# Kernel optimization log

Hardware: AMD Instinct MI355X
Metric: run time of the kernel (lower is better)

## Reference

```python
import jax, jax.numpy as jnp
import numpy as np

N_NODES = 100000
N_EDGES = 1600000
D_IN = 256
D_OUT = 256


def setup_inputs() -> dict:
    key = jax.random.key(0)
    k1, k2, k3, k4, k5 = jax.random.split(key, 5)
    feat = jax.random.normal(k1, (N_NODES, D_IN), dtype=jnp.float32)
    src = jax.random.randint(k2, (N_EDGES,), 0, N_NODES, dtype=jnp.int32)
    dst = jax.random.randint(k3, (N_EDGES,), 0, N_NODES, dtype=jnp.int32)
    # xavier_uniform with gain for relu (sqrt(2)), as in reset_parameters
    gain = float(np.sqrt(2.0))
    limit = gain * float(np.sqrt(6.0 / (D_IN + D_OUT)))
    w_neigh = jax.random.uniform(k4, (D_OUT, D_IN), minval=-limit, maxval=limit, dtype=jnp.float32)
    w_self = jax.random.uniform(k5, (D_OUT, D_IN), minval=-limit, maxval=limit, dtype=jnp.float32)
    b_self = jnp.zeros((D_OUT,), dtype=jnp.float32)
    return {"feat": feat, "src": src, "dst": dst,
            "w_neigh": w_neigh, "w_self": w_self, "b_self": b_self}


def reference(feat, src, dst, w_neigh, w_self, b_self):
    # SAGEConv, aggregator_type='mean', feat_drop=0, no edge_weight.
    # lin_before_mp = (in_feats > out_feats) = False -> aggregate raw feats first.
    n = feat.shape[0]
    # gather messages at edges and segment-sum into dst nodes
    summed = jax.ops.segment_sum(feat[src], dst, num_segments=n)  # [N, D_in]
    deg = jax.ops.segment_sum(jnp.ones_like(dst, dtype=feat.dtype), dst, num_segments=n)
    h_neigh_raw = summed / jnp.maximum(deg, 1.0)[:, None]  # mean; 0 for isolated nodes
    h_neigh = h_neigh_raw @ w_neigh.T                       # fc_neigh (no bias)
    rst = feat @ w_self.T + b_self + h_neigh                # fc_self(h_self) + h_neigh
    return rst
```

## Files before the change

kernel.cpp:

```cpp
#include <hip/hip_runtime.h>
#include <cstddef>

#define N_NODES 100000
#define N_EDGES 1600000
#define D 256

typedef short          s16x8 __attribute__((ext_vector_type(8)));
typedef unsigned short u16x8 __attribute__((ext_vector_type(8)));
typedef float          f32x4 __attribute__((ext_vector_type(4)));
typedef float          f32x8 __attribute__((ext_vector_type(8)));

__device__ __forceinline__ unsigned short f2bf(float f) {
    unsigned int u = __float_as_uint(f);
    unsigned int r = (u + 0x7fffu + ((u >> 16) & 1u)) >> 16;
    return (unsigned short)r;
}
__device__ __forceinline__ float bf2f(unsigned short u) {
    return __uint_as_float(((unsigned int)u) << 16);
}

#define WS_COUNTS 0
#define WS_ROWPTR (N_NODES)
#define WS_COL    (2 * N_NODES + 16)
#define WS_PART   (WS_COL + N_EDGES)
#define WB_BYTE   ((size_t)(WS_PART + 128) * 4)
#define FB_BYTE   (WB_BYTE + 2 * 65536 * 2)
#define FB_SZ     ((size_t)N_NODES * D * 2)
#define FQ_BYTE   FB_BYTE
#define FQ_SZ     ((size_t)N_NODES * D)
#define HB3_BYTE  (FQ_BYTE + FQ_SZ)
#define NEED_XL3  (HB3_BYTE + FB_SZ)
#define NEED_LARGE (FB_BYTE + FB_SZ)
#define NEED_MID  (FB_BYTE)

#define EBLOCKS ((N_EDGES + 255) / 256)
#define FBLOCKS (N_NODES * D / 8 / 256)
#define SCAN_NB ((N_NODES + 1023) / 1024)
#define GEMMBLKS ((N_NODES + 63) / 64)

__global__ __launch_bounds__(256) void cvt_hist_u8_kernel(
    const float* __restrict__ feat, const float* __restrict__ w_self,
    const float* __restrict__ w_neigh, const int* __restrict__ dst,
    unsigned char* __restrict__ fq, unsigned short* __restrict__ wb,
    int* __restrict__ counts)
{
    const int b = blockIdx.x;
    if (b < FBLOCKS) {
        const int i = b * 256 + threadIdx.x;
        const f32x8 v = ((const f32x8*)feat)[i];
        unsigned int p0 = 0, p1 = 0;
#pragma unroll
        for (int k = 0; k < 4; ++k) {
            int q = (int)rintf(fminf(fmaxf(v[k] * 16.0f, -127.0f), 127.0f)) + 128;
            p0 |= ((unsigned int)q) << (8 * k);
        }
#pragma unroll
        for (int k = 0; k < 4; ++k) {
            int q = (int)rintf(fminf(fmaxf(v[4 + k] * 16.0f, -127.0f), 127.0f)) + 128;
            p1 |= ((unsigned int)q) << (8 * k);
        }
        uint2 o; o.x = p0; o.y = p1;
        *(uint2*)(fq + (size_t)i * 8) = o;
    } else if (b < FBLOCKS + 128) {
        const int i = (b - FBLOCKS) * 256 + threadIdx.x;
        const bool isself = (i < 16384);
        const float* srcp = isself ? w_self : w_neigh;
        const int j = (isself ? i : i - 16384) * 4;
        const float4 v = *(const float4*)(srcp + j);
        ushort4 o;
        o.x = f2bf(v.x); o.y = f2bf(v.y); o.z = f2bf(v.z); o.w = f2bf(v.w);
        ((ushort4*)wb)[i] = o;
    } else {
        const int i = (b - FBLOCKS - 128) * 256 + threadIdx.x;
        if (i < N_EDGES) atomicAdd(&counts[dst[i]], 1);
    }
}

__global__ __launch_bounds__(256) void cvt_hist_bf16_kernel(
    const float* __restrict__ feat, const float* __restrict__ w_self,
    const float* __restrict__ w_neigh, const int* __restrict__ dst,
    unsigned short* __restrict__ fb, unsigned short* __restrict__ wb,
    int* __restrict__ counts)
{
    const int b = blockIdx.x;
    if (b < FBLOCKS) {
        const int i = b * 256 + threadIdx.x;
        const f32x8 v = ((const f32x8*)feat)[i];
        ushort4 a, c;
        a.x = f2bf(v[0]); a.y = f2bf(v[1]); a.z = f2bf(v[2]); a.w = f2bf(v[3]);
        c.x = f2bf(v[4]); c.y = f2bf(v[5]); c.z = f2bf(v[6]); c.w = f2bf(v[7]);
        ((ushort4*)fb)[i * 2 + 0] = a;
        ((ushort4*)fb)[i * 2 + 1] = c;
    } else if (b < FBLOCKS + 128) {
        const int i = (b - FBLOCKS) * 256 + threadIdx.x;
        const bool isself = (i < 16384);
        const float* srcp = isself ? w_self : w_neigh;
        const int j = (isself ? i : i - 16384) * 4;
        const float4 v = *(const float4*)(srcp + j);
        ushort4 o;
        o.x = f2bf(v.x); o.y = f2bf(v.y); o.z = f2bf(v.z); o.w = f2bf(v.w);
        ((ushort4*)wb)[i] = o;
    } else {
        const int i = (b - FBLOCKS - 128) * 256 + threadIdx.x;
        if (i < N_EDGES) atomicAdd(&counts[dst[i]], 1);
    }
}

__global__ __launch_bounds__(256) void wcvt_hist_kernel(
    const float* __restrict__ w_self, const float* __restrict__ w_neigh,
    const int* __restrict__ dst, unsigned short* __restrict__ wb,
    int* __restrict__ counts)
{
    const int b = blockIdx.x;
    if (b < 128) {
        const int i = b * 256 + threadIdx.x;
        const bool isself = (i < 16384);
        const float* srcp = isself ? w_self : w_neigh;
        const int j = (isself ? i : i - 16384) * 4;
        const float4 v = *(const float4*)(srcp + j);
        ushort4 o;
        o.x = f2bf(v.x); o.y = f2bf(v.y); o.z = f2bf(v.z); o.w = f2bf(v.w);
        ((ushort4*)wb)[i] = o;
    } else {
        const int i = (b - 128) * 256 + threadIdx.x;
        if (i < N_EDGES) atomicAdd(&counts[dst[i]], 1);
    }
}

__global__ __launch_bounds__(1024) void scan_block_kernel(
    const int* __restrict__ counts, int* __restrict__ row_ptr,
    int* __restrict__ partials)
{
    __shared__ int wsum[16];
    const int t = threadIdx.x, b = blockIdx.x, i = b * 1024 + t;
    const int lane = t & 63, w = t >> 6;
    int x = (i < N_NODES) ? counts[i] : 0;
#pragma unroll
    for (int off = 1; off < 64; off <<= 1) {
        int y = __shfl_up(x, off, 64);
        if (lane >= off) x += y;
    }
    if (lane == 63) wsum[w] = x;
    __syncthreads();
    if (w == 0) {
        int s = (lane < 16) ? wsum[lane] : 0;
#pragma unroll
        for (int off = 1; off < 16; off <<= 1) {
            int y = __shfl_up(s, off, 64);
            if (lane >= off) s += y;
        }
        if (lane < 16) wsum[lane] = s;
    }
    __syncthreads();
    const int incl = x + (w > 0 ? wsum[w - 1] : 0);
    if (i < N_NODES) row_ptr[i + 1] = incl;
    if (t == 1023) partials[b] = incl;
}

__global__ __launch_bounds__(1024) void scan_add2_kernel(
    const int* __restrict__ partials, int* __restrict__ row_ptr)
{
    __shared__ int sp[SCAN_NB];
    const int t = threadIdx.x, b = blockIdx.x;
    if (t < SCAN_NB) sp[t] = partials[t];
    __syncthreads();
    int off = 0;
    for (int j = 0; j < b; ++j) off += sp[j];
    const int i = b * 1024 + t;
    if (i < N_NODES) row_ptr[i + 1] += off;
    if (b == 0 && t == 0) row_ptr[0] = 0;
}

__global__ __launch_bounds__(256) void fill_kernel(
    const int* __restrict__ src, const int* __restrict__ dst,
    const int* __restrict__ row_ptr, int* __restrict__ counts,
    int* __restrict__ col)
{
    const int i = blockIdx.x * 256 + threadIdx.x;
    if (i < N_EDGES) {
        const int d = dst[i];
        const int pos = atomicSub(&counts[d], 1) - 1;
        col[row_ptr[d] + pos] = src[i];
    }
}

__global__ __launch_bounds__(256) void aggregate4_kernel(
    const unsigned char* __restrict__ fq,
    const int* __restrict__ row_ptr, const int* __restrict__ col,
    unsigned short* __restrict__ hb)
{
    const int node = (blockIdx.x * blockDim.x + threadIdx.x) >> 6;
    const int lane = threadIdx.x & 63;
    if (node >= N_NODES) return;
    const int beg = row_ptr[node], end = row_ptr[node + 1];
    const int quarter = lane >> 4;
    const int chunk = lane & 15;

    unsigned int aE[4] = {0,0,0,0}, aO[4] = {0,0,0,0};
    unsigned int bE[4] = {0,0,0,0}, bO[4] = {0,0,0,0};
    const unsigned char* base = fq + chunk * 16;

    int j = beg + quarter;
    for (; j + 4 < end; j += 8) {
        const int s0 = col[j];
        const int s1 = col[j + 4];
        const uint4 u = *(const uint4*)(base + (size_t)s0 * D);
        const uint4 v = *(const uint4*)(base + (size_t)s1 * D);
        aE[0] += u.x & 0x00FF00FFu;  aO[0] += (u.x >> 8) & 0x00FF00FFu;
        aE[1] += u.y & 0x00FF00FFu;  aO[1] += (u.y >> 8) & 0x00FF00FFu;
        aE[2] += u.z & 0x00FF00FFu;  aO[2] += (u.z >> 8) & 0x00FF00FFu;
        aE[3] += u.w & 0x00FF00FFu;  aO[3] += (u.w >> 8) & 0x00FF00FFu;
        bE[0] += v.x & 0x00FF00FFu;  bO[0] += (v.x >> 8) & 0x00FF00FFu;
        bE[1] += v.y & 0x00FF00FFu;  bO[1] += (v.y >> 8) & 0x00FF00FFu;
        bE[2] += v.z & 0x00FF00FFu;  bO[2] += (v.z >> 8) & 0x00FF00FFu;
        bE[3] += v.w & 0x00FF00FFu;  bO[3] += (v.w >> 8) & 0x00FF00FFu;
    }
    for (; j < end; j += 4) {
        const int s0 = col[j];
        const uint4 u = *(const uint4*)(base + (size_t)s0 * D);
        aE[0] += u.x & 0x00FF00FFu;  aO[0] += (u.x >> 8) & 0x00FF00FFu;
        aE[1] += u.y & 0x00FF00FFu;  aO[1] += (u.y >> 8) & 0x00FF00FFu;
        aE[2] += u.z & 0x00FF00FFu;  aO[2] += (u.z >> 8) & 0x00FF00FFu;
        aE[3] += u.w & 0x00FF00FFu;  aO[3] += (u.w >> 8) & 0x00FF00FFu;
    }

#pragma unroll
    for (int d = 0; d < 4; ++d) {
        unsigned int e = aE[d] + bE[d];
        unsigned int o = aO[d] + bO[d];
        e += __shfl_xor((int)e, 16, 64);
        e += __shfl_xor((int)e, 32, 64);
        o += __shfl_xor((int)o, 16, 64);
        o += __shfl_xor((int)o, 32, 64);
        aE[d] = e; aO[d] = o;
    }

    if (quarter == 0) {
        const int deg = end - beg;
        const float inv = 1.0f / (16.0f * fmaxf((float)deg, 1.0f));
        const float bias = 128.0f * (float)deg;
        u16x8 o0, o1;
#pragma unroll
        for (int d = 0; d < 4; ++d) {
            const float e0 = ((float)(aE[d] & 0xFFFFu) - bias) * inv;
            const float e2 = ((float)(aE[d] >> 16)     - bias) * inv;
            const float e1 = ((float)(aO[d] & 0xFFFFu) - bias) * inv;
            const float e3 = ((float)(aO[d] >> 16)     - bias) * inv;
            if (d < 2) {
                o0[d * 4 + 0] = f2bf(e0); o0[d * 4 + 1] = f2bf(e1);
                o0[d * 4 + 2] = f2bf(e2); o0[d * 4 + 3] = f2bf(e3);
            } else {
                o1[(d - 2) * 4 + 0] = f2bf(e0); o1[(d - 2) * 4 + 1] = f2bf(e1);
                o1[(d - 2) * 4 + 2] = f2bf(e2); o1[(d - 2) * 4 + 3] = f2bf(e3);
            }
        }
        unsigned short* op = hb + (size_t)node * D + chunk * 16;
        *(u16x8*)op = o0;
        *(u16x8*)(op + 8) = o1;
    }
}

__global__ __launch_bounds__(256) void gemm_v4_kernel(
    const float* __restrict__ feat,
    const unsigned short* __restrict__ hb,
    const unsigned short* __restrict__ wb,
    const float* __restrict__ b_self,
    float* __restrict__ outp)
{
    __shared__ unsigned short As[64 * 64];

    const int t    = threadIdx.x;
    const int lane = t & 63;
    const int w    = t >> 6;
    const int row0 = blockIdx.x * 64;
    const int c0   = w * 64;
    const int nl   = lane & 15;
    const int kg   = lane >> 4;

    const int tr = t >> 2;
    const int tq = t & 3;
    int grow = row0 + tr; if (grow > N_NODES - 1) grow = N_NODES - 1;
    const size_t gf = (size_t)grow * D;

    int wsw[2];
#pragma unroll
    for (int c = 0; c < 2; ++c) {
        const int cs = tq * 16 + c * 8;
        wsw[c] = tr * 64 + (cs ^ ((tr & 7) << 3));
    }
    int rsw[4][2];
#pragma unroll
    for (int m = 0; m < 4; ++m) {
        const int r = m * 16 + nl;
#pragma unroll
        for (int kk = 0; kk < 2; ++kk) {
            const int cs = kg * 8 + kk * 32;
            rsw[m][kk] = r * 64 + (cs ^ ((r & 7) << 3));
        }
    }

    f32x4 acc[4][4];
#pragma unroll
    for (int m = 0; m < 4; ++m)
#pragma unroll
        for (int n = 0; n < 4; ++n) acc[m][n] = (f32x4){0.f, 0.f, 0.f, 0.f};

    f32x8 stf0, stf1;
    u16x8 sth0, sth1;
    stf0 = *(const f32x8*)(feat + gf + tq * 16);
    stf1 = *(const f32x8*)(feat + gf + tq * 16 + 8);

#pragma unroll
    for (int s = 0; s < 8; ++s) {
        u16x8 w0, w1;
        if (s < 4) {
#pragma unroll
            for (int i = 0; i < 8; ++i) { w0[i] = f2bf(stf0[i]); w1[i] = f2bf(stf1[i]); }
        } else {
            w0 = sth0; w1 = sth1;
        }
        *(u16x8*)&As[wsw[0]] = w0;
        *(u16x8*)&As[wsw[1]] = w1;
        __syncthreads();

        if (s + 1 < 4) {
            const int koff = (s + 1) * 64 + tq * 16;
            stf0 = *(const f32x8*)(feat + gf + koff);
            stf1 = *(const f32x8*)(feat + gf + koff + 8);
        } else if (s + 1 < 8) {
            const int koff = ((s + 1) & 3) * 64 + tq * 16;
            sth0 = *(const u16x8*)(hb + gf + koff);
            sth1 = *(const u16x8*)(hb + gf + koff + 8);
        }

        const int hsel = (s < 4) ? 0 : 65536;
        const int kbase = (s & 3) * 64;
#pragma unroll
        for (int kk = 0; kk < 2; ++kk) {
            s16x8 a[4], b[4];
#pragma unroll
            for (int m = 0; m < 4; ++m)
                a[m] = *(const s16x8*)&As[rsw[m][kk]];
#pragma unroll
            for (int n = 0; n < 4; ++n)
                b[n] = *(const s16x8*)(wb + hsel
                        + (size_t)(c0 + n * 16 + nl) * 256 + kbase + kk * 32 + kg * 8);
#pragma unroll
            for (int m = 0; m < 4; ++m)
#pragma unroll
                for (int n = 0; n < 4; ++n)
                    acc[m][n] = __builtin_amdgcn_mfma_f32_16x16x32_bf16(
                        a[m], b[n], acc[m][n], 0, 0, 0);
        }
        __syncthreads();
    }

#pragma unroll
    for (int n = 0; n < 4; ++n) {
        const float bias = b_self[c0 + n * 16 + nl];
#pragma unroll
        for (int m = 0; m < 4; ++m) {
            const int rbase = row0 + m * 16 + kg * 4;
#pragma unroll
            for (int r = 0; r < 4; ++r) {
                const int row = rbase + r;
                if (row < N_NODES)
                    outp[(size_t)row * D + c0 + n * 16 + nl] = acc[m][n][r] + bias;
            }
        }
    }
}

__global__ __launch_bounds__(256) void aggregate2f_kernel(
    const unsigned short* __restrict__ featb,
    const int* __restrict__ row_ptr, const int* __restrict__ col,
    float* __restrict__ outf)
{
    const int node = (blockIdx.x * blockDim.x + threadIdx.x) >> 6;
    const int lane = threadIdx.x & 63;
    if (node >= N_NODES) return;
    const int beg = row_ptr[node], end = row_ptr[node + 1];
    const int half = lane >> 5;
    const int chunk = lane & 31;

    float a0[8] = {0,0,0,0,0,0,0,0};
    float a1[8] = {0,0,0,0,0,0,0,0};
    float a2[8] = {0,0,0,0,0,0,0,0};
    float a3[8] = {0,0,0,0,0,0,0,0};
    const unsigned short* fbp = featb + chunk * 8;

    int j = beg + half;
    for (; j + 6 < end; j += 8) {
        const int s0 = col[j], s1 = col[j + 2], s2 = col[j + 4], s3 = col[j + 6];
        const u16x8 u0 = *(const u16x8*)(fbp + (size_t)s0 * D);
        const u16x8 u1 = *(const u16x8*)(fbp + (size_t)s1 * D);
        const u16x8 u2 = *(const u16x8*)(fbp + (size_t)s2 * D);
        const u16x8 u3 = *(const u16x8*)(fbp + (size_t)s3 * D);
#pragma unroll
        for (int i = 0; i < 8; ++i) a0[i] += bf2f(u0[i]);
#pragma unroll
        for (int i = 0; i < 8; ++i) a1[i] += bf2f(u1[i]);
#pragma unroll
        for (int i = 0; i < 8; ++i) a2[i] += bf2f(u2[i]);
#pragma unroll
        for (int i = 0; i < 8; ++i) a3[i] += bf2f(u3[i]);
    }
    for (; j < end; j += 2) {
        const int s0 = col[j];
        const u16x8 u0 = *(const u16x8*)(fbp + (size_t)s0 * D);
#pragma unroll
        for (int i = 0; i < 8; ++i) a0[i] += bf2f(u0[i]);
    }

    const float invd = 1.0f / fmaxf((float)(end - beg), 1.0f);
    float tv[8];
#pragma unroll
    for (int i = 0; i < 8; ++i) {
        float v = (a0[i] + a1[i]) + (a2[i] + a3[i]);
        v += __shfl_xor(v, 32, 64);
        tv[i] = v * invd;
    }
    float4 o;
    o.x = tv[half * 4 + 0]; o.y = tv[half * 4 + 1];
    o.z = tv[half * 4 + 2]; o.w = tv[half * 4 + 3];
    *(float4*)(outf + (size_t)node * D + chunk * 8 + half * 4) = o;
}

__global__ __launch_bounds__(256) void aggregate_f32_kernel(
    const float* __restrict__ feat, const int* __restrict__ row_ptr,
    const int* __restrict__ col, float* __restrict__ outf)
{
    const int node = (blockIdx.x * blockDim.x + threadIdx.x) >> 6;
    const int lane = threadIdx.x & 63;
    if (node >= N_NODES) return;
    const int beg = row_ptr[node], end = row_ptr[node + 1];

    float4 a0 = make_float4(0.f, 0.f, 0.f, 0.f);
    float4 a1 = make_float4(0.f, 0.f, 0.f, 0.f);
    float4 a2 = make_float4(0.f, 0.f, 0.f, 0.f);
    float4 a3 = make_float4(0.f, 0.f, 0.f, 0.f);

#define ACC(acc, s)                                                          \
    do {                                                                     \
        const float4 v = ((const float4*)(feat + (size_t)(s) * D))[lane];    \
        acc.x += v.x; acc.y += v.y; acc.z += v.z; acc.w += v.w;              \
    } while (0)

    int j = beg;
    for (; j + 3 < end; j += 4) {
        const int s0 = col[j], s1 = col[j + 1], s2 = col[j + 2], s3 = col[j + 3];
        ACC(a0, s0); ACC(a1, s1); ACC(a2, s2); ACC(a3, s3);
    }
    for (; j < end; ++j) { const int s0 = col[j]; ACC(a0, s0); }
#undef ACC

    const float invd = 1.0f / fmaxf((float)(end - beg), 1.0f);
    float4 r;
    r.x = ((a0.x + a1.x) + (a2.x + a3.x)) * invd;
    r.y = ((a0.y + a1.y) + (a2.y + a3.y)) * invd;
    r.z = ((a0.z + a1.z) + (a2.z + a3.z)) * invd;
    r.w = ((a0.w + a1.w) + (a2.w + a3.w)) * invd;
    ((float4*)(outf + (size_t)node * D))[lane] = r;
}

__global__ __launch_bounds__(256) void gemm_mfma64_f32h_kernel(
    const float* __restrict__ feat,
    const unsigned short* __restrict__ wb,
    const float* __restrict__ b_self,
    const float* h32, float* outp)
{
    const int lane = threadIdx.x & 63;
    const int wslice = threadIdx.x >> 6;
    const int row0 = blockIdx.x * 64;
    const int c0 = wslice * 64;
    const int nl = lane & 15;
    const int kg = lane >> 4;

    f32x4 acc[4][4];
#pragma unroll
    for (int m = 0; m < 4; ++m)
#pragma unroll
        for (int n = 0; n < 4; ++n) acc[m][n] = (f32x4){0.f, 0.f, 0.f, 0.f};

    size_t aoff[4];
#pragma unroll
    for (int m = 0; m < 4; ++m) {
        int r = row0 + m * 16 + nl;
        if (r > N_NODES - 1) r = N_NODES - 1;
        aoff[m] = (size_t)r * D + kg * 8;
    }

#pragma unroll
    for (int hf = 0; hf < 2; ++hf) {
        const unsigned short* wh = wb + hf * 65536 + (size_t)(c0 + nl) * 256 + kg * 8;
#pragma unroll
        for (int kk = 0; kk < 8; ++kk) {
            const int kb = kk * 32;
            s16x8 afrag[4];
#pragma unroll
            for (int m = 0; m < 4; ++m) {
                const float* ap = hf == 0 ? (const float*)feat : h32;
                const f32x8 av = *(const f32x8*)(ap + aoff[m] + kb);
#pragma unroll
                for (int i = 0; i < 8; ++i) afrag[m][i] = (short)f2bf(av[i]);
            }
            s16x8 bfrag[4];
#pragma unroll
            for (int n = 0; n < 4; ++n)
                bfrag[n] = *(const s16x8*)(wh + n * 4096 + kb);
#pragma unroll
            for (int m = 0; m < 4; ++m)
#pragma unroll
                for (int n = 0; n < 4; ++n)
                    acc[m][n] = __builtin_amdgcn_mfma_f32_16x16x32_bf16(
                        afrag[m], bfrag[n], acc[m][n], 0, 0, 0);
        }
    }

    __syncthreads();

#pragma unroll
    for (int n = 0; n < 4; ++n) {
        const float bias = b_self[c0 + n * 16 + nl];
#pragma unroll
        for (int m = 0; m < 4; ++m) {
            const int rbase = row0 + m * 16 + kg * 4;
#pragma unroll
            for (int r = 0; r < 4; ++r) {
                const int row = rbase + r;
                if (row < N_NODES)
                    outp[(size_t)row * D + c0 + n * 16 + nl] = acc[m][n][r] + bias;
            }
        }
    }
}

__global__ __launch_bounds__(256) void scatter_kernel(
    const float* __restrict__ feat, const int* __restrict__ src,
    const int* __restrict__ dst, float* __restrict__ S, float* __restrict__ deg)
{
    const int gtid = blockIdx.x * blockDim.x + threadIdx.x;
    const int wave = gtid >> 6;
    const int lane = gtid & 63;
    const int nwaves = (gridDim.x * blockDim.x) >> 6;
    for (int e = wave; e < N_EDGES; e += nwaves) {
        const int s = src[e];
        const int d = dst[e];
        if (lane == 0) unsafeAtomicAdd(&deg[d], 1.0f);
        const float4 v = ((const float4*)(feat + (size_t)s * D))[lane];
        float* o = S + (size_t)d * D + lane * 4;
        unsafeAtomicAdd(o + 0, v.x);
        unsafeAtomicAdd(o + 1, v.y);
        unsafeAtomicAdd(o + 2, v.z);
        unsafeAtomicAdd(o + 3, v.w);
    }
}

#define BM 64
#define BK 16

__global__ __launch_bounds__(256) void fused_gemm_f32(
    const float* __restrict__ feat, const float* __restrict__ w_neigh,
    const float* __restrict__ w_self, const float* __restrict__ b_self,
    const float* __restrict__ deg, float* out)
{
    __shared__ float At[BK][BM + 4];
    __shared__ float Bt[BK][256];

    const int tid = threadIdx.x;
    const int i0 = blockIdx.x * BM;
    const int trow = tid >> 4;
    const int tcol = tid & 15;
    const int m_load = tid >> 2;
    const int kq = tid & 3;

    const int arow = i0 + m_load;
    const bool arow_ok = arow < N_NODES;
    float invd = 1.0f;
    if (arow_ok) invd = 1.0f / fmaxf(deg[arow], 1.0f);

    float acc[4][16];
#pragma unroll
    for (int r = 0; r < 4; ++r)
#pragma unroll
        for (int c = 0; c < 16; ++c) acc[r][c] = 0.0f;

    for (int kc = 0; kc < (2 * D) / BK; ++kc) {
        const int kb = kc * BK;
        const bool self_part = (kb < D);
        const int kbase = self_part ? kb : (kb - D);

        float4 va = make_float4(0.f, 0.f, 0.f, 0.f);
        if (arow_ok) {
            const float* ap = self_part ? feat : out;
            va = *(const float4*)(ap + (size_t)arow * D + kbase + kq * 4);
            if (!self_part) { va.x *= invd; va.y *= invd; va.z *= invd; va.w *= invd; }
        }
        const float* W = self_part ? w_self : w_neigh;
        const float4* wp = (const float4*)(W + (size_t)tid * D + kbase);
        const float4 w0 = wp[0], w1 = wp[1], w2 = wp[2], w3 = wp[3];

        __syncthreads();
        At[kq * 4 + 0][m_load] = va.x;
        At[kq * 4 + 1][m_load] = va.y;
        At[kq * 4 + 2][m_load] = va.z;
        At[kq * 4 + 3][m_load] = va.w;
        Bt[ 0][tid] = w0.x; Bt[ 1][tid] = w0.y; Bt[ 2][tid] = w0.z; Bt[ 3][tid] = w0.w;
        Bt[ 4][tid] = w1.x; Bt[ 5][tid] = w1.y; Bt[ 6][tid] = w1.z; Bt[ 7][tid] = w1.w;
        Bt[ 8][tid] = w2.x; Bt[ 9][tid] = w2.y; Bt[10][tid] = w2.z; Bt[11][tid] = w2.w;
        Bt[12][tid] = w3.x; Bt[13][tid] = w3.y; Bt[14][tid] = w3.z; Bt[15][tid] = w3.w;
        __syncthreads();

#pragma unroll
        for (int k = 0; k < BK; ++k) {
            const float4 a = *(const float4*)&At[k][trow * 4];
            float4 b[4];
#pragma unroll
            for (int g = 0; g < 4; ++g)
                b[g] = *(const float4*)&Bt[k][g * 64 + tcol * 4];
            const float av[4] = {a.x, a.y, a.z, a.w};
#pragma unroll
            for (int r = 0; r < 4; ++r)
#pragma unroll
                for (int g = 0; g < 4; ++g) {
                    acc[r][g * 4 + 0] = fmaf(av[r], b[g].x, acc[r][g * 4 + 0]);
                    acc[r][g * 4 + 1] = fmaf(av[r], b[g].y, acc[r][g * 4 + 1]);
                    acc[r][g * 4 + 2] = fmaf(av[r], b[g].z, acc[r][g * 4 + 2]);
                    acc[r][g * 4 + 3] = fmaf(av[r], b[g].w, acc[r][g * 4 + 3]);
                }
        }
    }

    float4 bias[4];
#pragma unroll
    for (int g = 0; g < 4; ++g)
        bias[g] = *(const float4*)&b_self[g * 64 + tcol * 4];

#pragma unroll
    for (int r = 0; r < 4; ++r) {
        const int row = i0 + trow * 4 + r;
        if (row < N_NODES) {
            float* op = out + (size_t)row * D;
#pragma unroll
            for (int g = 0; g < 4; ++g) {
                float4 v;
                v.x = acc[r][g * 4 + 0] + bias[g].x;
                v.y = acc[r][g * 4 + 1] + bias[g].y;
                v.z = acc[r][g * 4 + 2] + bias[g].z;
                v.w = acc[r][g * 4 + 3] + bias[g].w;
                *(float4*)(op + g * 64 + tcol * 4) = v;
            }
        }
    }
}

extern "C" void kernel_launch(void* const* d_in, const int* in_sizes, int n_in,
                              void* d_out, int out_size, void* d_ws, size_t ws_size,
                              hipStream_t stream) {
    const float* feat    = (const float*)d_in[0];
    const int*   src     = (const int*)d_in[1];
    const int*   dst     = (const int*)d_in[2];
    const float* w_neigh = (const float*)d_in[3];
    const float* w_self  = (const float*)d_in[4];
    const float* b_self  = (const float*)d_in[5];
    float* out = (float*)d_out;

    const int ablocks = (N_NODES * 64 + 255) / 256;

    if (ws_size >= NEED_MID) {
        int* wsI     = (int*)d_ws;
        int* counts  = wsI + WS_COUNTS;
        int* row_ptr = wsI + WS_ROWPTR;
        int* col     = wsI + WS_COL;
        int* part    = wsI + WS_PART;
        unsigned short* wb = (unsigned short*)((char*)d_ws + WB_BYTE);
        unsigned short* fb = (unsigned short*)((char*)d_ws + FB_BYTE);
        unsigned char*  fq = (unsigned char*)((char*)d_ws + FQ_BYTE);
        unsigned short* hb = (unsigned short*)((char*)d_ws + HB3_BYTE);

        hipMemsetAsync(counts, 0, N_NODES * sizeof(int), stream);
        if (ws_size >= NEED_XL3)
            cvt_hist_u8_kernel<<<FBLOCKS + 128 + EBLOCKS, 256, 0, stream>>>(
                feat, w_self, w_neigh, dst, fq, wb, counts);
        else if (ws_size >= NEED_LARGE)
            cvt_hist_bf16_kernel<<<FBLOCKS + 128 + EBLOCKS, 256, 0, stream>>>(
                feat, w_self, w_neigh, dst, fb, wb, counts);
        else
            wcvt_hist_kernel<<<128 + EBLOCKS, 256, 0, stream>>>(
                w_self, w_neigh, dst, wb, counts);
        scan_block_kernel<<<SCAN_NB, 1024, 0, stream>>>(counts, row_ptr, part);
        scan_add2_kernel<<<SCAN_NB, 1024, 0, stream>>>(part, row_ptr);
        fill_kernel<<<EBLOCKS, 256, 0, stream>>>(src, dst, row_ptr, counts, col);

        if (ws_size >= NEED_XL3) {
            aggregate4_kernel<<<ablocks, 256, 0, stream>>>(fq, row_ptr, col, hb);
            gemm_v4_kernel<<<GEMMBLKS, 256, 0, stream>>>(feat, hb, wb, b_self, out);
        } else if (ws_size >= NEED_LARGE) {
            aggregate2f_kernel<<<ablocks, 256, 0, stream>>>(
                fb, row_ptr, col, out);
            gemm_mfma64_f32h_kernel<<<GEMMBLKS, 256, 0, stream>>>(
                feat, wb, b_self, out, out);
        } else {
            aggregate_f32_kernel<<<ablocks, 256, 0, stream>>>(
                feat, row_ptr, col, out);
            gemm_mfma64_f32h_kernel<<<GEMMBLKS, 256, 0, stream>>>(
                feat, wb, b_self, out, out);
        }
    } else {
        float* deg = (float*)d_ws;
        hipMemsetAsync(out, 0, (size_t)N_NODES * D * sizeof(float), stream);
        hipMemsetAsync(deg, 0, (size_t)N_NODES * sizeof(float), stream);
        scatter_kernel<<<4096, 256, 0, stream>>>(feat, src, dst, out, deg);
        fused_gemm_f32<<<(N_NODES + BM - 1) / BM, 256, 0, stream>>>(
            feat, w_neigh, w_self, b_self, deg, out);
    }
}
```

Baseline: 367.3 us.

## Slice histogram and CSR fill by destination range to localize atomics

Splits the degree histogram out of the conversion kernel into its own kernel. Both the histogram and the CSR fill are rewritten so that each block handles one chunk of edges and only the destinations falling in one of 8 node-range slices. Adjacent blocks therefore work on the same edge chunk but different slices, which confines the scattered atomics and col writes to a smaller address range so they stay in cache. The cost is that dst (and src in the fill) is read 8 times, and one extra kernel launch is added.

After: 349.1 us. -5.0%, faster.

```diff
diff --git a/kernel.cpp b/kernel.cpp
--- a/kernel.cpp
+++ b/kernel.cpp
@@ -33,16 +33,19 @@
 #define NEED_LARGE (FB_BYTE + FB_SZ)
 #define NEED_MID  (FB_BYTE)
 
-#define EBLOCKS ((N_EDGES + 255) / 256)
 #define FBLOCKS (N_NODES * D / 8 / 256)
 #define SCAN_NB ((N_NODES + 1023) / 1024)
 #define GEMMBLKS ((N_NODES + 63) / 64)
-
-__global__ __launch_bounds__(256) void cvt_hist_u8_kernel(
+#define NSLICE 8
+#define SLICE_N (N_NODES / NSLICE)
+#define ECHUNK 2048
+#define ECHUNKS ((N_EDGES + ECHUNK - 1) / ECHUNK)
+#define SLICED_NB (ECHUNKS * NSLICE)
+
+__global__ __launch_bounds__(256) void cvt_u8_kernel(
     const float* __restrict__ feat, const float* __restrict__ w_self,
-    const float* __restrict__ w_neigh, const int* __restrict__ dst,
-    unsigned char* __restrict__ fq, unsigned short* __restrict__ wb,
-    int* __restrict__ counts)
+    const float* __restrict__ w_neigh,
+    unsigned char* __restrict__ fq, unsigned short* __restrict__ wb)
 {
     const int b = blockIdx.x;
     if (b < FBLOCKS) {
@@ -61,7 +64,7 @@
         }
         uint2 o; o.x = p0; o.y = p1;
         *(uint2*)(fq + (size_t)i * 8) = o;
-    } else if (b < FBLOCKS + 128) {
+    } else {
         const int i = (b - FBLOCKS) * 256 + threadIdx.x;
         const bool isself = (i < 16384);
         const float* srcp = isself ? w_self : w_neigh;
@@ -70,17 +73,13 @@
         ushort4 o;
         o.x = f2bf(v.x); o.y = f2bf(v.y); o.z = f2bf(v.z); o.w = f2bf(v.w);
         ((ushort4*)wb)[i] = o;
-    } else {
-        const int i = (b - FBLOCKS - 128) * 256 + threadIdx.x;
-        if (i < N_EDGES) atomicAdd(&counts[dst[i]], 1);
-    }
-}
-
-__global__ __launch_bounds__(256) void cvt_hist_bf16_kernel(
+    }
+}
+
+__global__ __launch_bounds__(256) void cvt_bf16_kernel(
     const float* __restrict__ feat, const float* __restrict__ w_self,
-    const float* __restrict__ w_neigh, const int* __restrict__ dst,
-    unsigned short* __restrict__ fb, unsigned short* __restrict__ wb,
-    int* __restrict__ counts)
+    const float* __restrict__ w_neigh,
+    unsigned short* __restrict__ fb, unsigned short* __restrict__ wb)
 {
     const int b = blockIdx.x;
     if (b < FBLOCKS) {
@@ -91,7 +90,7 @@
         c.x = f2bf(v[4]); c.y = f2bf(v[5]); c.z = f2bf(v[6]); c.w = f2bf(v[7]);
         ((ushort4*)fb)[i * 2 + 0] = a;
         ((ushort4*)fb)[i * 2 + 1] = c;
-    } else if (b < FBLOCKS + 128) {
+    } else {
         const int i = (b - FBLOCKS) * 256 + threadIdx.x;
         const bool isself = (i < 16384);
         const float* srcp = isself ? w_self : w_neigh;
@@ -100,30 +99,43 @@
         ushort4 o;
         o.x = f2bf(v.x); o.y = f2bf(v.y); o.z = f2bf(v.z); o.w = f2bf(v.w);
         ((ushort4*)wb)[i] = o;
+    }
+}
+
+__global__ __launch_bounds__(256) void wcvt_kernel(
+    const float* __restrict__ w_self, const float* __restrict__ w_neigh,
+    unsigned short* __restrict__ wb)
+{
+    const int i = blockIdx.x * 256 + threadIdx.x;
+    const bool isself = (i < 16384);
+    const float* srcp = isself ? w_self : w_neigh;
+    const int j = (isself ? i : i - 16384) * 4;
+    const float4 v = *(const float4*)(srcp + j);
+    ushort4 o;
+    o.x = f2bf(v.x); o.y = f2bf(v.y); o.z = f2bf(v.z); o.w = f2bf(v.w);
+    ((ushort4*)wb)[i] = o;
+}
+
+__global__ __launch_bounds__(256) void hist_sliced_kernel(
+    const int* __restrict__ dst, int* __restrict__ counts)
+{
+    const int slice = blockIdx.x & (NSLICE - 1);
+    const int chunk = blockIdx.x >> 3;
+    const int lo = slice * SLICE_N, hi = lo + SLICE_N;
+    const int e0 = chunk * ECHUNK + threadIdx.x * 8;
+    if (e0 >= N_EDGES) return;
+    if (e0 + 8 <= N_EDGES) {
+        const int4 d0 = *(const int4*)(dst + e0);
+        const int4 d1 = *(const int4*)(dst + e0 + 4);
+        const int dv[8] = {d0.x, d0.y, d0.z, d0.w, d1.x, d1.y, d1.z, d1.w};
+#pragma unroll
+        for (int k = 0; k < 8; ++k)
+            if (dv[k] >= lo && dv[k] < hi) atomicAdd(&counts[dv[k]], 1);
     } else {
-        const int i = (b - FBLOCKS - 128) * 256 + threadIdx.x;
-        if (i < N_EDGES) atomicAdd(&counts[dst[i]], 1);
-    }
-}
-
-__global__ __launch_bounds__(256) void wcvt_hist_kernel(
-    const float* __restrict__ w_self, const float* __restrict__ w_neigh,
-    const int* __restrict__ dst, unsigned short* __restrict__ wb,
-    int* __restrict__ counts)
-{
-    const int b = blockIdx.x;
-    if (b < 128) {
-        const int i = b * 256 + threadIdx.x;
-        const bool isself = (i < 16384);
-        const float* srcp = isself ? w_self : w_neigh;
-        const int j = (isself ? i : i - 16384) * 4;
-        const float4 v = *(const float4*)(srcp + j);
-        ushort4 o;
-        o.x = f2bf(v.x); o.y = f2bf(v.y); o.z = f2bf(v.z); o.w = f2bf(v.w);
-        ((ushort4*)wb)[i] = o;
-    } else {
-        const int i = (b - 128) * 256 + threadIdx.x;
-        if (i < N_EDGES) atomicAdd(&counts[dst[i]], 1);
+        for (int e = e0; e < N_EDGES; ++e) {
+            const int d = dst[e];
+            if (d >= lo && d < hi) atomicAdd(&counts[d], 1);
+        }
     }
 }
 
@@ -171,16 +183,39 @@
     if (b == 0 && t == 0) row_ptr[0] = 0;
 }
 
-__global__ __launch_bounds__(256) void fill_kernel(
+__global__ __launch_bounds__(256) void fill_sliced_kernel(
     const int* __restrict__ src, const int* __restrict__ dst,
     const int* __restrict__ row_ptr, int* __restrict__ counts,
     int* __restrict__ col)
 {
-    const int i = blockIdx.x * 256 + threadIdx.x;
-    if (i < N_EDGES) {
-        const int d = dst[i];
-        const int pos = atomicSub(&counts[d], 1) - 1;
-        col[row_ptr[d] + pos] = src[i];
+    const int slice = blockIdx.x & (NSLICE - 1);
+    const int chunk = blockIdx.x >> 3;
+    const int lo = slice * SLICE_N, hi = lo + SLICE_N;
+    const int e0 = chunk * ECHUNK + threadIdx.x * 8;
+    if (e0 >= N_EDGES) return;
+    if (e0 + 8 <= N_EDGES) {
+        const int4 d0 = *(const int4*)(dst + e0);
+        const int4 d1 = *(const int4*)(dst + e0 + 4);
+        const int4 s0 = *(const int4*)(src + e0);
+        const int4 s1 = *(const int4*)(src + e0 + 4);
+        const int dv[8] = {d0.x, d0.y, d0.z, d0.w, d1.x, d1.y, d1.z, d1.w};
+        const int sv[8] = {s0.x, s0.y, s0.z, s0.w, s1.x, s1.y, s1.z, s1.w};
+#pragma unroll
+        for (int k = 0; k < 8; ++k) {
+            const int d = dv[k];
+            if (d >= lo && d < hi) {
+                const int pos = atomicSub(&counts[d], 1) - 1;
+                col[row_ptr[d] + pos] = sv[k];
+            }
+        }
+    } else {
+        for (int e = e0; e < N_EDGES; ++e) {
+            const int d = dst[e];
+            if (d >= lo && d < hi) {
+                const int pos = atomicSub(&counts[d], 1) - 1;
+                col[row_ptr[d] + pos] = src[e];
+            }
+        }
     }
 }
 
@@ -680,17 +715,19 @@
 
         hipMemsetAsync(counts, 0, N_NODES * sizeof(int), stream);
         if (ws_size >= NEED_XL3)
-            cvt_hist_u8_kernel<<<FBLOCKS + 128 + EBLOCKS, 256, 0, stream>>>(
-                feat, w_self, w_neigh, dst, fq, wb, counts);
+            cvt_u8_kernel<<<FBLOCKS + 128, 256, 0, stream>>>(
+                feat, w_self, w_neigh, fq, wb);
         else if (ws_size >= NEED_LARGE)
-            cvt_hist_bf16_kernel<<<FBLOCKS + 128 + EBLOCKS, 256, 0, stream>>>(
-                feat, w_self, w_neigh, dst, fb, wb, counts);
+            cvt_bf16_kernel<<<FBLOCKS + 128, 256, 0, stream>>>(
+                feat, w_self, w_neigh, fb, wb);
         else
-            wcvt_hist_kernel<<<128 + EBLOCKS, 256, 0, stream>>>(
-                w_self, w_neigh, dst, wb, counts);
+            wcvt_kernel<<<128, 256, 0, stream>>>(w_self, w_neigh, wb);
+
+        hist_sliced_kernel<<<SLICED_NB, 256, 0, stream>>>(dst, counts);
         scan_block_kernel<<<SCAN_NB, 1024, 0, stream>>>(counts, row_ptr, part);
         scan_add2_kernel<<<SCAN_NB, 1024, 0, stream>>>(part, row_ptr);
-        fill_kernel<<<EBLOCKS, 256, 0, stream>>>(src, dst, row_ptr, counts, col);
+        fill_sliced_kernel<<<SLICED_NB, 256, 0, stream>>>(
+            src, dst, row_ptr, counts, col);
 
         if (ws_size >= NEED_XL3) {
             aggregate4_kernel<<<ablocks, 256, 0, stream>>>(fq, row_ptr, col, hb);
```
